# Performance work log

Measured on AMD Instinct MI355X. Metric: run time of the kernel, lower is better.

Reference implementation:

```python
import jax, jax.numpy as jnp
import numpy as np

B, L, H = 64, 512, 400          # batch, seq_len, encoder hidden (HeadSentinel(400))
EN, EL, NLAB = 256, 128, 128    # edge-node dim, edge-label hidden, num head_tags


def setup_inputs():
    key = jax.random.key(0)
    ks = jax.random.split(key, 16)
    g = lambda k, shape, s=0.05: jax.random.normal(k, shape, jnp.float32) * s
    return dict(
        memory_bank=jax.random.normal(ks[0], (B, L, H), jnp.float32),
        edge_heads=jax.random.randint(ks[1], (B, L), 0, L + 1, jnp.int32),
        edge_labels=jax.random.randint(ks[2], (B, L), 0, NLAB, jnp.int32),
        corefs=jax.random.randint(ks[3], (B, L), 0, L, jnp.int32),
        mask=jnp.ones((B, L), jnp.int32),
        sentinel=g(ks[4], (H,)),
        W_enh=g(ks[5], (H, EN)), b_enh=jnp.zeros((EN,), jnp.float32),
        W_enm=g(ks[6], (H, EN)), b_enm=jnp.zeros((EN,), jnp.float32),
        W_elh=g(ks[7], (H, EL)), b_elh=jnp.zeros((EL,), jnp.float32),
        W_elm=g(ks[8], (H, EL)), b_elm=jnp.zeros((EL,), jnp.float32),
        ba_U=g(ks[9], (EN, EN)), ba_Wd=g(ks[10], (EN,)), ba_We=g(ks[11], (EN,)),
        ba_b=jnp.zeros((), jnp.float32),
        lbl_U=g(ks[12], (NLAB, EL, EL)), lbl_Wl=g(ks[13], (NLAB, EL)),
        lbl_Wr=g(ks[14], (NLAB, EL)), lbl_b=jnp.zeros((NLAB,), jnp.float32),
    )


def _label_scores(elh_sel, elm, lbl_U, lbl_Wl, lbl_Wr, lbl_b):
    # Bilinear label scorer: [B, L1, NLAB]
    return (jnp.einsum('bld,nde,ble->bln', elh_sel, lbl_U, elm)
            + elh_sel @ lbl_Wl.T + elm @ lbl_Wr.T + lbl_b)


def reference(memory_bank, edge_heads, edge_labels, corefs, mask, sentinel,
              W_enh, b_enh, W_enm, b_enm, W_elh, b_elh, W_elm, b_elm,
              ba_U, ba_Wd, ba_We, ba_b, lbl_U, lbl_Wl, lbl_Wr, lbl_b):
    elu = jax.nn.elu
    Bsz = memory_bank.shape[0]
    # ---- add head sentinel (mask/heads/labels get a leading zero column) ----
    mb = jnp.concatenate([jnp.broadcast_to(sentinel, (Bsz, 1, sentinel.shape[0])), memory_bank], 1)
    z = jnp.zeros((Bsz, 1), jnp.int32)
    heads1 = jnp.concatenate([z, edge_heads], 1)    # [B, L1]
    labels1 = jnp.concatenate([z, edge_labels], 1)  # [B, L1]
    mask1 = jnp.concatenate([z, mask], 1)           # [B, L1]
    L1 = mb.shape[1]
    # ---- encode (Dropout is identity at inference) ----
    enh = elu(mb @ W_enh + b_enh)
    enm = elu(mb @ W_enm + b_enm)
    elh = elu(mb @ W_elh + b_elh)
    elm = elu(mb @ W_elm + b_elm)
    # ---- biaffine edge-node scores: s[b, head, mod] ----
    node_scores = (jnp.einsum('bhd,de,bme->bhm', enh, ba_U, enm)
                   + (enh @ ba_Wd)[:, :, None] + (enm @ ba_We)[:, None, :] + ba_b)
    # ---- loss ----
    mask2 = (mask1[:, :, None] + mask1[:, None, :]).astype(jnp.float32)
    node_ll = jax.nn.log_softmax(node_scores + jnp.log(mask2 + 1e-45), axis=1)
    elh_gold = jnp.take_along_axis(elh, heads1[:, :, None], axis=1)  # gather_nd(create_indices)
    lbl_ll = jax.nn.log_softmax(_label_scores(elh_gold, elm, lbl_U, lbl_Wl, lbl_Wr, lbl_b), axis=2)
    gold_node_ll = jnp.take_along_axis(node_ll, heads1[:, None, :], axis=1)[:, 0, :]  # ll[b, head[b,m], m]
    gold_lbl_ll = jnp.take_along_axis(lbl_ll, labels1[:, :, None], axis=2)[:, :, 0]   # ll[b, m, label[b,m]]
    node_nll = -jnp.sum(gold_node_ll[:, 1:])
    label_nll = -jnp.sum(gold_lbl_ll[:, 1:])
    # ---- decode ----
    dec = node_scores + jnp.diag(jnp.full((L1,), -jnp.inf))
    mm = (1.0 - mask1.astype(jnp.float32)) * (-1e8)
    dec = dec + mm[:, :, None] + mm[:, None, :]
    pred_heads = jnp.argmax(dec, axis=1)                              # [B, L1]
    elh_pred = jnp.take_along_axis(elh, pred_heads[:, :, None], axis=1)
    pred_lbl = jnp.max(_label_scores(elh_pred, elm, lbl_U, lbl_Wl, lbl_Wr, lbl_b), axis=2)
    return (pred_heads[:, 1:].astype(jnp.float32), pred_lbl[:, 1:],
            labels1.astype(jnp.float32), node_nll, label_nll)
```

## Files before the change

### kernel.cpp

```cpp
#include <hip/hip_runtime.h>
#include <hip/hip_bf16.h>

#define BB 64
#define LLEN 512
#define HH 400
#define L1 513
#define TT 32832
#define NE 768
#define KP 16640
#define PHW 4160
#define KPAD 416

typedef __attribute__((ext_vector_type(4))) float f32x4;
typedef __attribute__((ext_vector_type(8))) short bf16x8;
typedef unsigned int u32;
typedef __attribute__((address_space(1))) const u32* gptr_t;
typedef __attribute__((address_space(3))) u32* sptr_t;

__device__ inline unsigned short f2bf(float x){
  unsigned u = __float_as_uint(x);
  unsigned r = (u + 0x7fffu + ((u >> 16) & 1u)) >> 16;
  return (unsigned short)r;
}
__device__ inline unsigned cvtpk(float a, float b){
  unsigned r;
  asm("v_cvt_pk_bf16_f32 %0, %1, %2" : "=v"(r) : "v"(a), "v"(b));
  return r;
}
__device__ inline float bf2f(unsigned short h){
  return __uint_as_float(((unsigned)h) << 16);
}

__global__ __launch_bounds__(256) void k_init(const int* eh, const int* el, float* out,
                                              int* idx, int* labbuf){
  int t = blockIdx.x*256 + threadIdx.x;
  if (t < TT){
    int b = t / L1, m = t - b*L1;
    int lab = m ? el[b*LLEN + m - 1] : 0;
    int hd  = m ? eh[b*LLEN + m - 1] : 0;
    out[65536 + t] = (float)lab;
    labbuf[t] = lab;
    idx[t] = b*L1 + hd;
  }
  if (blockIdx.x == 0 && threadIdx.x < 2) out[98368 + threadIdx.x] = 0.f;
}

__global__ __launch_bounds__(256) void k_wcat(const float* Wenh,const float* benh,
    const float* Wenm,const float* benm,const float* Welh,const float* belh,
    const float* Welm,const float* belm, unsigned short* WH, unsigned short* WL,
    float* bcat){
  int g = blockIdx.x*256 + threadIdx.x;
  if (g < NE*KPAD){
    int n = g / KPAD, k = g - n*KPAD;
    float v = 0.f;
    if (k < HH){
      if (n < 256) v = Wenh[k*256 + n];
      else if (n < 512) v = Wenm[k*256 + n - 256];
      else if (n < 640) v = Welh[k*128 + n - 512];
      else v = Welm[k*128 + n - 640];
    }
    unsigned short h = f2bf(v);
    WH[g] = h;
    WL[g] = f2bf(v - bf2f(h));
  }
  if (g < NE){
    float v;
    if (g < 256) v = benh[g];
    else if (g < 512) v = benm[g - 256];
    else if (g < 640) v = belh[g - 512];
    else v = belm[g - 640];
    bcat[g] = v;
  }
}

__global__ __launch_bounds__(256) void k_wu(const float* baU, unsigned short* UH,
    unsigned short* UL){
  int g = blockIdx.x*256 + threadIdx.x;
  int n = g >> 8, k = g & 255;
  float v = baU[k*256 + n];
  unsigned short h = f2bf(v);
  UH[g] = h;
  UL[g] = f2bf(v - bf2f(h));
}

__global__ __launch_bounds__(256) void k_wtt(const float* lblU, const float* Wl,
    const float* Wr, unsigned short* WtTp){
  int n = blockIdx.y;
  int kp = blockIdx.x*256 + threadIdx.x;
  if (kp >= KP) return;
  int p = kp / PHW; int q2 = kp - p*PHW; int dd = q2 >> 5; int j = q2 & 31; int e = p*32 + j;
  float v;
  if (dd < 128) v = lblU[(size_t)n*16384 + dd*128 + e];
  else if (dd == 128) v = Wl[n*128 + e];
  else v = Wr[n*128 + e];
  WtTp[(size_t)n*KP + kp] = f2bf(v);
}

__global__ __launch_bounds__(512) void k_encm(const float* mb, const float* sent,
    const unsigned short* WH, const unsigned short* WL, const float* bcat, float* E){
  __shared__ __align__(16) unsigned char Bst[2][2][8192];
  int tid = threadIdx.x, w = tid >> 6, lane = tid & 63, c = lane & 15, q = lane >> 4;
  int tb0 = blockIdx.x*256 + w*32;
  int n0 = blockIdx.y*128;

  const float* ap[2];
  #pragma unroll
  for (int ms = 0; ms < 2; ms++){
    int row = tb0 + ms*16 + c;
    const float* p = sent;
    if (row < TT){
      int br = row / L1, mr = row - br*L1;
      if (mr) p = mb + (size_t)(br*LLEN + mr - 1)*HH;
    }
    ap[ms] = p;
  }

  int f = tid;
  int bn = ((f >> 6) << 4) + (f & 15);
  int bkq = (f >> 4) & 3;
  const char* srcH = (const char*)WH + (size_t)(n0 + bn)*(KPAD*2) + bkq*16;
  const char* srcL = (const char*)WL + (size_t)(n0 + bn)*(KPAD*2) + bkq*16;
  auto stageB = [&](int s){
    __builtin_amdgcn_global_load_lds((gptr_t)(srcH + (size_t)s*64),
        (sptr_t)(&Bst[s & 1][0][f*16]), 16, 0, 0);
    __builtin_amdgcn_global_load_lds((gptr_t)(srcL + (size_t)s*64),
        (sptr_t)(&Bst[s & 1][1][f*16]), 16, 0, 0);
  };

  float4 a0[2], a1[2];
  auto loadA = [&](int s){
    #pragma unroll
    for (int ms = 0; ms < 2; ms++){
      int k = s*32 + q*8;
      float4 v0 = make_float4(0.f,0.f,0.f,0.f), v1 = v0;
      if (k < HH){ v0 = *(const float4*)(ap[ms] + k); v1 = *(const float4*)(ap[ms] + k + 4); }
      a0[ms] = v0; a1[ms] = v1;
    }
  };
  stageB(0);
  loadA(0);

  f32x4 acc[2][8];
  #pragma unroll
  for (int ms = 0; ms < 2; ms++)
    #pragma unroll
    for (int ns = 0; ns < 8; ns++){ acc[ms][ns][0]=0.f; acc[ms][ns][1]=0.f; acc[ms][ns][2]=0.f; acc[ms][ns][3]=0.f; }

  for (int s = 0; s < 13; s++){
    asm volatile("s_waitcnt vmcnt(0)" ::: "memory");
    __builtin_amdgcn_sched_barrier(0);
    __builtin_amdgcn_s_barrier();
    __builtin_amdgcn_sched_barrier(0);
    if (s + 1 < 13) stageB(s + 1);
    bf16x8 Ah[2], Al[2];
    #pragma unroll
    for (int ms = 0; ms < 2; ms++){
      float v[8] = {a0[ms].x,a0[ms].y,a0[ms].z,a0[ms].w,a1[ms].x,a1[ms].y,a1[ms].z,a1[ms].w};
      union { unsigned u[4]; bf16x8 b; } uh, ul;
      float r[8];
      #pragma unroll
      for (int j = 0; j < 4; j++){
        unsigned h = cvtpk(v[2*j], v[2*j+1]);
        uh.u[j] = h;
        r[2*j]   = v[2*j]   - __uint_as_float((h & 0xffffu) << 16);
        r[2*j+1] = v[2*j+1] - __uint_as_float((h >> 16) << 16);
      }
      #pragma unroll
      for (int j = 0; j < 4; j++) ul.u[j] = cvtpk(r[2*j], r[2*j+1]);
      Ah[ms] = uh.b; Al[ms] = ul.b;
    }
    if (s + 1 < 13) loadA(s + 1);
    const char* bh = (const char*)&Bst[s & 1][0][0];
    const char* bl = (const char*)&Bst[s & 1][1][0];
    #pragma unroll
    for (int ns = 0; ns < 8; ns++){
      bf16x8 BH = *(const bf16x8*)(bh + ns*1024 + lane*16);
      bf16x8 BL = *(const bf16x8*)(bl + ns*1024 + lane*16);
      #pragma unroll
      for (int ms = 0; ms < 2; ms++){
        acc[ms][ns] = __builtin_amdgcn_mfma_f32_16x16x32_bf16(Ah[ms], BH, acc[ms][ns], 0, 0, 0);
        acc[ms][ns] = __builtin_amdgcn_mfma_f32_16x16x32_bf16(Ah[ms], BL, acc[ms][ns], 0, 0, 0);
        acc[ms][ns] = __builtin_amdgcn_mfma_f32_16x16x32_bf16(Al[ms], BH, acc[ms][ns], 0, 0, 0);
      }
    }
  }

  float bvv[8];
  #pragma unroll
  for (int ns = 0; ns < 8; ns++) bvv[ns] = bcat[n0 + ns*16 + c];
  #pragma unroll
  for (int ms = 0; ms < 2; ms++){
    #pragma unroll
    for (int i = 0; i < 4; i++){
      int row = tb0 + ms*16 + 4*q + i;
      if (row < TT){
        #pragma unroll
        for (int ns = 0; ns < 8; ns++){
          float t = acc[ms][ns][i] + bvv[ns];
          E[(size_t)row*NE + n0 + ns*16 + c] = t > 0.f ? t : expm1f(t);
        }
      }
    }
  }
}

__global__ __launch_bounds__(256) void k_t1m(const float* E, const unsigned short* UH,
    const unsigned short* UL, float* T1){
  __shared__ __align__(16) unsigned char Bst[2][2][8192];
  int tid = threadIdx.x, w = tid >> 6, lane = tid & 63, c = lane & 15, q = lane >> 4;
  int tb0 = blockIdx.x*128 + w*32;
  int n0 = blockIdx.y*128;

  const float* ap[2];
  #pragma unroll
  for (int ms = 0; ms < 2; ms++){
    int row = tb0 + ms*16 + c;
    ap[ms] = E + (size_t)(row < TT ? row : 0)*NE;
  }

  auto stageB = [&](int s){
    #pragma unroll
    for (int i = 0; i < 2; i++){
      int f = i*256 + tid;
      int n = n0 + ((f >> 6) << 4) + (f & 15);
      int kq = (f >> 4) & 3;
      __builtin_amdgcn_global_load_lds((gptr_t)((const char*)UH + (size_t)n*512 + (size_t)s*64 + kq*16),
          (sptr_t)(&Bst[s & 1][0][f*16]), 16, 0, 0);
      __builtin_amdgcn_global_load_lds((gptr_t)((const char*)UL + (size_t)n*512 + (size_t)s*64 + kq*16),
          (sptr_t)(&Bst[s & 1][1][f*16]), 16, 0, 0);
    }
  };

  float4 a0[2], a1[2];
  auto loadA = [&](int s){
    #pragma unroll
    for (int ms = 0; ms < 2; ms++){
      int k = s*32 + q*8;
      a0[ms] = *(const float4*)(ap[ms] + k);
      a1[ms] = *(const float4*)(ap[ms] + k + 4);
    }
  };
  stageB(0);
  loadA(0);

  f32x4 acc[2][8];
  #pragma unroll
  for (int ms = 0; ms < 2; ms++)
    #pragma unroll
    for (int ns = 0; ns < 8; ns++){ acc[ms][ns][0]=0.f; acc[ms][ns][1]=0.f; acc[ms][ns][2]=0.f; acc[ms][ns][3]=0.f; }

  for (int s = 0; s < 8; s++){
    asm volatile("s_waitcnt vmcnt(0)" ::: "memory");
    __builtin_amdgcn_sched_barrier(0);
    __builtin_amdgcn_s_barrier();
    __builtin_amdgcn_sched_barrier(0);
    if (s + 1 < 8) stageB(s + 1);
    bf16x8 Ah[2], Al[2];
    #pragma unroll
    for (int ms = 0; ms < 2; ms++){
      float v[8] = {a0[ms].x,a0[ms].y,a0[ms].z,a0[ms].w,a1[ms].x,a1[ms].y,a1[ms].z,a1[ms].w};
      union { unsigned u[4]; bf16x8 b; } uh, ul;
      float r[8];
      #pragma unroll
      for (int j = 0; j < 4; j++){
        unsigned h = cvtpk(v[2*j], v[2*j+1]);
        uh.u[j] = h;
        r[2*j]   = v[2*j]   - __uint_as_float((h & 0xffffu) << 16);
        r[2*j+1] = v[2*j+1] - __uint_as_float((h >> 16) << 16);
      }
      #pragma unroll
      for (int j = 0; j < 4; j++) ul.u[j] = cvtpk(r[2*j], r[2*j+1]);
      Ah[ms] = uh.b; Al[ms] = ul.b;
    }
    if (s + 1 < 8) loadA(s + 1);
    const char* bh = (const char*)&Bst[s & 1][0][0];
    const char* bl = (const char*)&Bst[s & 1][1][0];
    #pragma unroll
    for (int ns = 0; ns < 8; ns++){
      bf16x8 BH = *(const bf16x8*)(bh + ns*1024 + lane*16);
      bf16x8 BL = *(const bf16x8*)(bl + ns*1024 + lane*16);
      #pragma unroll
      for (int ms = 0; ms < 2; ms++){
        acc[ms][ns] = __builtin_amdgcn_mfma_f32_16x16x32_bf16(Ah[ms], BH, acc[ms][ns], 0, 0, 0);
        acc[ms][ns] = __builtin_amdgcn_mfma_f32_16x16x32_bf16(Ah[ms], BL, acc[ms][ns], 0, 0, 0);
        acc[ms][ns] = __builtin_amdgcn_mfma_f32_16x16x32_bf16(Al[ms], BH, acc[ms][ns], 0, 0, 0);
      }
    }
  }

  #pragma unroll
  for (int ms = 0; ms < 2; ms++){
    #pragma unroll
    for (int i = 0; i < 4; i++){
      int row = tb0 + ms*16 + 4*q + i;
      if (row < TT){
        #pragma unroll
        for (int ns = 0; ns < 8; ns++)
          T1[(size_t)row*256 + n0 + ns*16 + c] = acc[ms][ns][i];
      }
    }
  }
}

__global__ __launch_bounds__(256) void k_vecs(const float* E, const float* Wd,
    const float* We, const float* bab, float* dvec, float* evec){
  int w = threadIdx.x >> 6, lane = threadIdx.x & 63;
  int t = blockIdx.x*4 + w;
  const float* enh = E + (size_t)t*NE;
  const float* enm = enh + 256;
  float sd = 0.f, se = 0.f;
  for (int l = lane; l < 256; l += 64){ sd += enh[l]*Wd[l]; se += enm[l]*We[l]; }
  for (int o = 1; o < 64; o <<= 1){ sd += __shfl_xor(sd, o, 64); se += __shfl_xor(se, o, 64); }
  if (lane == 0){ dvec[t] = sd + bab[0]; evec[t] = se; }
}

__global__ __launch_bounds__(256) void k_nsm(const float* T1, const float* E,
    const float* dvec, const float* evec, float* S){
  __shared__ __align__(16) unsigned char Bst[2][2][8192];
  int tid = threadIdx.x, w = tid >> 6, lane = tid & 63, c = lane & 15, q = lane >> 4;
  int b = blockIdx.y;
  int tm = blockIdx.x / 5, tn = blockIdx.x - tm*5;
  int Mb = tm*128, n0 = tn*128;
  int tb0 = Mb + w*32;

  const float* ap[2];
  #pragma unroll
  for (int ms = 0; ms < 2; ms++){
    int h = tb0 + ms*16 + c;
    int hc = h < L1 ? h : L1 - 1;
    ap[ms] = T1 + ((size_t)b*L1 + hc)*256;
  }

  auto stageB = [&](int s, int buf){
    int k0 = s*32;
    #pragma unroll
    for (int i = 0; i < 2; i++){
      int f = i*256 + tid;
      int mc = n0 + ((f >> 6) << 4) + (f & 15);
      int kq = (f >> 4) & 3;
      int mcc = mc < L1 ? mc : L1 - 1;
      const float* src = E + ((size_t)b*L1 + mcc)*NE + 256 + k0 + kq*8;
      float4 v0 = *(const float4*)src;
      float4 v1 = *(const float4*)(src + 4);
      float v[8] = {v0.x,v0.y,v0.z,v0.w,v1.x,v1.y,v1.z,v1.w};
      union { unsigned u[4]; uint4 u4; } uh, ul;
      float r[8];
      #pragma unroll
      for (int j = 0; j < 4; j++){
        unsigned h = cvtpk(v[2*j], v[2*j+1]);
        uh.u[j] = h;
        r[2*j]   = v[2*j]   - __uint_as_float((h & 0xffffu) << 16);
        r[2*j+1] = v[2*j+1] - __uint_as_float((h >> 16) << 16);
      }
      #pragma unroll
      for (int j = 0; j < 4; j++) ul.u[j] = cvtpk(r[2*j], r[2*j+1]);
      *(uint4*)&Bst[buf][0][f*16] = uh.u4;
      *(uint4*)&Bst[buf][1][f*16] = ul.u4;
    }
  };

  float4 a0[2], a1[2];
  auto loadA = [&](int s){
    #pragma unroll
    for (int ms = 0; ms < 2; ms++){
      int k = s*32 + q*8;
      a0[ms] = *(const float4*)(ap[ms] + k);
      a1[ms] = *(const float4*)(ap[ms] + k + 4);
    }
  };

  stageB(0, 0);
  loadA(0);

  f32x4 acc[2][8];
  #pragma unroll
  for (int ms = 0; ms < 2; ms++)
    #pragma unroll
    for (int ns = 0; ns < 8; ns++){ acc[ms][ns][0]=0.f; acc[ms][ns][1]=0.f; acc[ms][ns][2]=0.f; acc[ms][ns][3]=0.f; }

  __syncthreads();

  for (int s = 0; s < 8; s++){
    if (s + 1 < 8) stageB(s + 1, (s + 1) & 1);
    bf16x8 Ah[2], Al[2];
    #pragma unroll
    for (int ms = 0; ms < 2; ms++){
      float v[8] = {a0[ms].x,a0[ms].y,a0[ms].z,a0[ms].w,a1[ms].x,a1[ms].y,a1[ms].z,a1[ms].w};
      union { unsigned u[4]; bf16x8 b; } uh, ul;
      float r[8];
      #pragma unroll
      for (int j = 0; j < 4; j++){
        unsigned h = cvtpk(v[2*j], v[2*j+1]);
        uh.u[j] = h;
        r[2*j]   = v[2*j]   - __uint_as_float((h & 0xffffu) << 16);
        r[2*j+1] = v[2*j+1] - __uint_as_float((h >> 16) << 16);
      }
      #pragma unroll
      for (int j = 0; j < 4; j++) ul.u[j] = cvtpk(r[2*j], r[2*j+1]);
      Ah[ms] = uh.b; Al[ms] = ul.b;
    }
    if (s + 1 < 8) loadA(s + 1);
    const char* bh = (const char*)&Bst[s & 1][0][0];
    const char* bl = (const char*)&Bst[s & 1][1][0];
    #pragma unroll
    for (int ns = 0; ns < 8; ns++){
      bf16x8 BH = *(const bf16x8*)(bh + ns*1024 + lane*16);
      bf16x8 BL = *(const bf16x8*)(bl + ns*1024 + lane*16);
      #pragma unroll
      for (int ms = 0; ms < 2; ms++){
        acc[ms][ns] = __builtin_amdgcn_mfma_f32_16x16x32_bf16(Ah[ms], BH, acc[ms][ns], 0, 0, 0);
        acc[ms][ns] = __builtin_amdgcn_mfma_f32_16x16x32_bf16(Ah[ms], BL, acc[ms][ns], 0, 0, 0);
        acc[ms][ns] = __builtin_amdgcn_mfma_f32_16x16x32_bf16(Al[ms], BH, acc[ms][ns], 0, 0, 0);
      }
    }
    __syncthreads();
  }

  float er[8];
  #pragma unroll
  for (int ns = 0; ns < 8; ns++){
    int m = n0 + ns*16 + c;
    er[ns] = (m < L1) ? evec[b*L1 + m] : 0.f;
  }
  float* Sb = S + (size_t)b*L1*L1;
  #pragma unroll
  for (int ms = 0; ms < 2; ms++){
    #pragma unroll
    for (int i = 0; i < 4; i++){
      int h = tb0 + ms*16 + 4*q + i;
      if (h < L1){
        float dv = dvec[b*L1 + h];
        #pragma unroll
        for (int ns = 0; ns < 8; ns++){
          int m = n0 + ns*16 + c;
          if (m < L1) Sb[(size_t)h*L1 + m] = acc[ms][ns][i] + dv + er[ns];
        }
      }
    }
  }
}

__global__ __launch_bounds__(256) void k_nodecol(const float* S, const int* eh,
    const int* mask, float* out, int* idx){
  int b = blockIdx.y, mt = blockIdx.x;
  __shared__ float msk[L1];
  __shared__ float rM[8][32], rS[8][32], rG[8][32], rB[8][32];
  __shared__ int rH[8][32];
  __shared__ float npart[32];
  int tid = threadIdx.x; int c = tid & 31, r = tid >> 5;
  for (int h = tid; h < L1; h += 256) msk[h] = h ? (float)mask[b*LLEN + h - 1] : 0.f;
  __syncthreads();
  int m = mt*32 + c; bool valid = m < L1; int mc = valid ? m : (L1-1);
  float maskm = msk[mc];
  int gold = 0; if (valid && m) gold = eh[b*LLEN + m - 1];
  const float* Sb = S + (size_t)b*L1*L1;
  float Mx = -3.4e38f, Sm = 0.f, G = 0.f, Bv = -3.4e38f; int Bh = 0;
  for (int h = r; h < L1; h += 8){
    float s = Sb[(size_t)h*L1 + mc];
    float adj = s + ((msk[h] + maskm) > 1.5f ? 0.69314718055994531f : 0.f);
    float nm = fmaxf(Mx, adj);
    Sm = Sm * expf(Mx - nm) + expf(adj - nm);
    Mx = nm;
    if (h == gold) G = adj;
    float dv = (h == m) ? -3.4e38f : (s + (msk[h] > 0.5f ? 0.f : -1e8f));
    if (dv > Bv){ Bv = dv; Bh = h; }
  }
  rM[r][c] = Mx; rS[r][c] = Sm; rG[r][c] = G; rB[r][c] = Bv; rH[r][c] = Bh;
  __syncthreads();
  if (r == 0){
    float M0 = rM[0][c], S0 = rS[0][c], G0 = rG[0][c], B0 = rB[0][c]; int H0 = rH[0][c];
    for (int rr = 1; rr < 8; rr++){
      float m2 = rM[rr][c], s2 = rS[rr][c];
      float nm = fmaxf(M0, m2);
      S0 = S0*expf(M0 - nm) + s2*expf(m2 - nm); M0 = nm;
      G0 += rG[rr][c];
      float b2 = rB[rr][c]; int h2 = rH[rr][c];
      if (b2 > B0 || (b2 == B0 && h2 < H0)){ B0 = b2; H0 = h2; }
    }
    float nll = 0.f;
    if (valid && m >= 1) nll = (M0 + logf(S0)) - G0;
    npart[c] = nll;
    if (valid){
      idx[TT + b*L1 + m] = b*L1 + H0;
      if (m >= 1) out[b*LLEN + m - 1] = (float)H0;
    }
  }
  __syncthreads();
  if (tid == 0){
    float ssum = 0.f;
    for (int i2 = 0; i2 < 32; i2++) ssum += npart[i2];
    atomicAdd(out + 98368, ssum);
  }
}

__global__ __launch_bounds__(512, 1) void k_label(const float* E, const unsigned short* WtTp,
    const int* idx, const int* labbuf, const float* lblb, float* out){
  __shared__ __align__(16) unsigned char Bst[8*8192];
  __shared__ __align__(16) unsigned int xls[256*65];
  int tid = threadIdx.x;
  int w = tid >> 6, lane = tid & 63, c = lane & 15, q = lane >> 4;
  int wgrp = w & 3, khalf = w >> 2;
  int bx = blockIdx.x;
  bool pred = bx >= 128;
  int q0 = (bx & 127) * 256;
  int ibase = pred ? TT : 0;

  const char* gW = (const char*)WtTp;
  int f = tid;
  int bn = ((f >> 6) << 4) + (f & 15);
  int bkq = (f >> 4) & 3;
  const char* bsrc0 = gW + (size_t)bn*(KP*2) + (size_t)bkq*16;
  unsigned char* BbA = Bst;
  unsigned char* BbB = Bst + 4*8192;
  auto stage2 = [&](int s){
    __builtin_amdgcn_global_load_lds((gptr_t)(bsrc0 + (size_t)s*64),
        (sptr_t)(BbA + (s & 3)*8192 + f*16), 16, 0, 0);
    __builtin_amdgcn_global_load_lds((gptr_t)(bsrc0 + (size_t)(260 + s)*64),
        (sptr_t)(BbB + (s & 3)*8192 + f*16), 16, 0, 0);
  };
  stage2(0); stage2(1);

  {
    int tok = tid >> 1, half = tid & 1;
    int qq = q0 + tok;
    int trow = (qq >> 9)*L1 + (qq & 511) + 1;
    int g = idx[ibase + trow];
    const float* xr = E + (size_t)g*NE + 512 + half*64;
    unsigned* dstx = &xls[tok*65 + half*32];
    #pragma unroll
    for (int j = 0; j < 16; j++){
      float4 v = *(const float4*)(xr + j*4);
      dstx[2*j]   = cvtpk(v.x, v.y);
      dstx[2*j+1] = cvtpk(v.z, v.w);
    }
  }

  const float *yvb[4], *xvb[4];
  int tokl[4];
  #pragma unroll
  for (int ms = 0; ms < 4; ms++){
    int tl = (wgrp*4 + ms)*16 + c;
    tokl[ms] = tl;
    int qq = q0 + tl;
    int trow = (qq >> 9)*L1 + (qq & 511) + 1;
    int g = idx[ibase + trow];
    yvb[ms] = E + (size_t)trow*NE + 640 + 8*q;
    xvb[ms] = E + (size_t)g*NE + 512 + 8*q;
  }
  f32x4 acc[4][8];
  #pragma unroll
  for (int ms = 0; ms < 4; ms++)
    #pragma unroll
    for (int ns = 0; ns < 8; ns++){ acc[ms][ns][0]=0.f; acc[ms][ns][1]=0.f; acc[ms][ns][2]=0.f; acc[ms][ns][3]=0.f; }

  __syncthreads();

  const unsigned short* xsh = (const unsigned short*)xls;
  float xs0[4], xs1[4];
  #pragma unroll
  for (int ms = 0; ms < 4; ms++){
    xs0[ms] = bf2f(xsh[tokl[ms]*130]);
    xs1[ms] = bf2f(xsh[tokl[ms]*130 + 1]);
  }

  float yreg[4][8];
  for (int u = 0; u < 130; u++){
    if (u) { asm volatile("s_waitcnt vmcnt(0)" ::: "memory"); }
    __builtin_amdgcn_sched_barrier(0);
    __builtin_amdgcn_s_barrier();
    __builtin_amdgcn_sched_barrier(0);
    if (2*u + 2 < 260){ stage2(2*u + 2); stage2(2*u + 3); }
    int ph = (u >= 65);
    int d0 = 2*u - ph*130;
    if (d0 == 0){
      int e0 = (khalf*2 + ph) * 32;
      #pragma unroll
      for (int ms = 0; ms < 4; ms++){
        float4 v0 = *(const float4*)(yvb[ms] + e0);
        float4 v1 = *(const float4*)(yvb[ms] + e0 + 4);
        yreg[ms][0]=v0.x; yreg[ms][1]=v0.y; yreg[ms][2]=v0.z; yreg[ms][3]=v0.w;
        yreg[ms][4]=v1.x; yreg[ms][5]=v1.y; yreg[ms][6]=v1.z; yreg[ms][7]=v1.w;
      }
    }
    bf16x8 afr0[4], afr1[4];
    if (d0 < 128){
      #pragma unroll
      for (int ms = 0; ms < 4; ms++){
        float a0 = xs0[ms], a1 = xs1[ms];
        union { unsigned u[4]; bf16x8 v; } u0, u1;
        u0.u[0] = cvtpk(a0*yreg[ms][0], a0*yreg[ms][1]);
        u0.u[1] = cvtpk(a0*yreg[ms][2], a0*yreg[ms][3]);
        u0.u[2] = cvtpk(a0*yreg[ms][4], a0*yreg[ms][5]);
        u0.u[3] = cvtpk(a0*yreg[ms][6], a0*yreg[ms][7]);
        u1.u[0] = cvtpk(a1*yreg[ms][0], a1*yreg[ms][1]);
        u1.u[1] = cvtpk(a1*yreg[ms][2], a1*yreg[ms][3]);
        u1.u[2] = cvtpk(a1*yreg[ms][4], a1*yreg[ms][5]);
        u1.u[3] = cvtpk(a1*yreg[ms][6], a1*yreg[ms][7]);
        afr0[ms] = u0.v; afr1[ms] = u1.v;
      }
    } else {
      int e0 = (khalf*2 + ph) * 32;
      #pragma unroll
      for (int ms = 0; ms < 4; ms++){
        float4 u0f = *(const float4*)(xvb[ms] + e0);
        float4 u1f = *(const float4*)(xvb[ms] + e0 + 4);
        union { unsigned u[4]; bf16x8 v; } ux, uy;
        ux.u[0]=cvtpk(u0f.x,u0f.y); ux.u[1]=cvtpk(u0f.z,u0f.w);
        ux.u[2]=cvtpk(u1f.x,u1f.y); ux.u[3]=cvtpk(u1f.z,u1f.w);
        uy.u[0]=cvtpk(yreg[ms][0],yreg[ms][1]); uy.u[1]=cvtpk(yreg[ms][2],yreg[ms][3]);
        uy.u[2]=cvtpk(yreg[ms][4],yreg[ms][5]); uy.u[3]=cvtpk(yreg[ms][6],yreg[ms][7]);
        afr0[ms] = ux.v; afr1[ms] = uy.v;
      }
    }
    {
      int nd0 = 2*(u + 1) - ((u + 1 >= 65) ? 130 : 0);
      if (nd0 >= 128) nd0 = 0;
      #pragma unroll
      for (int ms = 0; ms < 4; ms++){
        xs0[ms] = bf2f(xsh[tokl[ms]*130 + nd0]);
        xs1[ms] = bf2f(xsh[tokl[ms]*130 + nd0 + 1]);
      }
    }
    const char* hb = (const char*)(khalf ? BbB : BbA);
    const char* bs0 = hb + ((2*u) & 3)*8192;
    const char* bs1 = hb + ((2*u + 1) & 3)*8192;
    #pragma unroll
    for (int ns = 0; ns < 8; ns++){
      bf16x8 bfr0 = *(const bf16x8*)(bs0 + ns*1024 + lane*16);
      bf16x8 bfr1 = *(const bf16x8*)(bs1 + ns*1024 + lane*16);
      #pragma unroll
      for (int ms = 0; ms < 4; ms++){
        acc[ms][ns] = __builtin_amdgcn_mfma_f32_16x16x32_bf16(afr0[ms], bfr0, acc[ms][ns], 0, 0, 0);
        acc[ms][ns] = __builtin_amdgcn_mfma_f32_16x16x32_bf16(afr1[ms], bfr1, acc[ms][ns], 0, 0, 0);
      }
    }
  }

  __syncthreads();
  float* cmb = (float*)xls;
  #pragma unroll
  for (int ms = 0; ms < 4; ms++){
    if (khalf == 1){
      #pragma unroll
      for (int ns = 0; ns < 8; ns++)
        *(f32x4*)&cmb[((wgrp*64 + lane)*8 + ((ns + lane) & 7))*4] = acc[ms][ns];
    }
    __syncthreads();
    if (khalf == 0){
      #pragma unroll
      for (int ns = 0; ns < 8; ns++){
        f32x4 t = *(const f32x4*)&cmb[((wgrp*64 + lane)*8 + ((ns + lane) & 7))*4];
        acc[ms][ns][0] += t[0]; acc[ms][ns][1] += t[1];
        acc[ms][ns][2] += t[2]; acc[ms][ns][3] += t[3];
      }
    }
    __syncthreads();
  }
  if (khalf == 1) return;

  float bv[8];
  #pragma unroll
  for (int ns = 0; ns < 8; ns++) bv[ns] = lblb[ns*16 + c];
  float part = 0.f;
  #pragma unroll
  for (int ms = 0; ms < 4; ms++){
    int tb = (wgrp*4 + ms)*16 + 4*q;
    float mx[4] = {-3.4e38f, -3.4e38f, -3.4e38f, -3.4e38f};
    #pragma unroll
    for (int ns = 0; ns < 8; ns++)
      #pragma unroll
      for (int i = 0; i < 4; i++){
        float v = acc[ms][ns][i] + bv[ns];
        mx[i] = fmaxf(mx[i], v);
      }
    #pragma unroll
    for (int o = 1; o < 16; o <<= 1)
      #pragma unroll
      for (int i = 0; i < 4; i++) mx[i] = fmaxf(mx[i], __shfl_xor(mx[i], o, 64));
    if (!pred){
      int lab[4];
      #pragma unroll
      for (int i = 0; i < 4; i++){
        int qq = q0 + tb + i;
        int trow = (qq >> 9)*L1 + (qq & 511) + 1;
        lab[i] = labbuf[trow];
      }
      float se[4] = {0.f,0.f,0.f,0.f}, gp[4] = {0.f,0.f,0.f,0.f};
      #pragma unroll
      for (int ns = 0; ns < 8; ns++)
        #pragma unroll
        for (int i = 0; i < 4; i++){
          float v = acc[ms][ns][i] + bv[ns];
          se[i] += expf(v - mx[i]);
          if (ns*16 + c == lab[i]) gp[i] += v;
        }
      #pragma unroll
      for (int o = 1; o < 16; o <<= 1)
        #pragma unroll
        for (int i = 0; i < 4; i++){ se[i] += __shfl_xor(se[i], o, 64); gp[i] += __shfl_xor(gp[i], o, 64); }
      if (c == 0){
        #pragma unroll
        for (int i = 0; i < 4; i++) part += mx[i] + logf(se[i]) - gp[i];
      }
    } else {
      if (c == 0){
        #pragma unroll
        for (int i = 0; i < 4; i++)
          out[32768 + q0 + tb + i] = mx[i];
      }
    }
  }
  if (!pred){
    for (int o = 1; o < 64; o <<= 1) part += __shfl_xor(part, o, 64);
    if (lane == 0) atomicAdd(out + 98369, part);
  }
}

extern "C" void kernel_launch(void* const* d_in, const int* in_sizes, int n_in,
                              void* d_out, int out_size, void* d_ws, size_t ws_size,
                              hipStream_t stream){
  const float* memory_bank = (const float*)d_in[0];
  const int* edge_heads = (const int*)d_in[1];
  const int* edge_labels = (const int*)d_in[2];
  const int* mask = (const int*)d_in[4];
  const float* sentinel = (const float*)d_in[5];
  const float* W_enh = (const float*)d_in[6];  const float* b_enh = (const float*)d_in[7];
  const float* W_enm = (const float*)d_in[8];  const float* b_enm = (const float*)d_in[9];
  const float* W_elh = (const float*)d_in[10]; const float* b_elh = (const float*)d_in[11];
  const float* W_elm = (const float*)d_in[12]; const float* b_elm = (const float*)d_in[13];
  const float* ba_U = (const float*)d_in[14];  const float* ba_Wd = (const float*)d_in[15];
  const float* ba_We = (const float*)d_in[16]; const float* ba_b = (const float*)d_in[17];
  const float* lbl_U = (const float*)d_in[18]; const float* lbl_Wl = (const float*)d_in[19];
  const float* lbl_Wr = (const float*)d_in[20]; const float* lbl_b = (const float*)d_in[21];
  float* out = (float*)d_out;

  char* wsc = (char*)d_ws;
  size_t o = 0;
  auto alloc = [&](size_t n){ o = (o + 255) & ~(size_t)255; void* pp = wsc + o; o += n; return pp; };
  float* E     = (float*)alloc((size_t)TT*NE*4);
  float* T1    = (float*)alloc((size_t)TT*256*4);
  float* S     = (float*)alloc((size_t)BB*L1*L1*4);
  unsigned short* WH = (unsigned short*)alloc((size_t)NE*KPAD*2);
  unsigned short* WL = (unsigned short*)alloc((size_t)NE*KPAD*2);
  unsigned short* UH = (unsigned short*)alloc((size_t)256*256*2);
  unsigned short* UL = (unsigned short*)alloc((size_t)256*256*2);
  float* bcat  = (float*)alloc((size_t)NE*4);
  unsigned short* WtTp = (unsigned short*)alloc((size_t)128*KP*2);
  float* dvec  = (float*)alloc((size_t)TT*4);
  float* evec  = (float*)alloc((size_t)TT*4);
  int*   idx   = (int*)alloc((size_t)2*TT*4);
  int*   labbuf= (int*)alloc((size_t)TT*4);

  k_init<<<dim3(129), 256, 0, stream>>>(edge_heads, edge_labels, out, idx, labbuf);
  k_wcat<<<dim3(1248), 256, 0, stream>>>(W_enh, b_enh, W_enm, b_enm, W_elh, b_elh, W_elm, b_elm, WH, WL, bcat);
  k_wu<<<dim3(256), 256, 0, stream>>>(ba_U, UH, UL);
  k_wtt<<<dim3(65, 128), 256, 0, stream>>>(lbl_U, lbl_Wl, lbl_Wr, WtTp);
  k_encm<<<dim3(129, 6), 512, 0, stream>>>(memory_bank, sentinel, WH, WL, bcat, E);
  k_t1m<<<dim3(257, 2), 256, 0, stream>>>(E, UH, UL, T1);
  k_vecs<<<dim3(8208), 256, 0, stream>>>(E, ba_Wd, ba_We, ba_b, dvec, evec);
  k_nsm<<<dim3(25, 64), 256, 0, stream>>>(T1, E, dvec, evec, S);
  k_nodecol<<<dim3(17, 64), 256, 0, stream>>>(S, edge_heads, mask, out, idx);
  k_label<<<dim3(256), 512, 0, stream>>>(E, WtTp, idx, labbuf, lbl_b, out);
}
```

Before: 699.9 us.

## Fuse d/e vector dots into encoder epilogue and transpose score matrix for column reductions

```diff
diff --git a/kernel.cpp b/kernel.cpp
--- a/kernel.cpp
+++ b/kernel.cpp
@@ -32,7 +32,8 @@
 }
 
 __global__ __launch_bounds__(256) void k_init(const int* eh, const int* el, float* out,
-                                              int* idx, int* labbuf){
+                                              int* idx, int* labbuf, const float* bab,
+                                              float* dvec, float* evec){
   int t = blockIdx.x*256 + threadIdx.x;
   if (t < TT){
     int b = t / L1, m = t - b*L1;
@@ -41,6 +42,8 @@
     out[65536 + t] = (float)lab;
     labbuf[t] = lab;
     idx[t] = b*L1 + hd;
+    dvec[t] = bab[0];
+    evec[t] = 0.f;
   }
   if (blockIdx.x == 0 && threadIdx.x < 2) out[98368 + threadIdx.x] = 0.f;
 }
@@ -97,7 +100,8 @@
 }
 
 __global__ __launch_bounds__(512) void k_encm(const float* mb, const float* sent,
-    const unsigned short* WH, const unsigned short* WL, const float* bcat, float* E){
+    const unsigned short* WH, const unsigned short* WL, const float* bcat,
+    const float* Wd, const float* We, float* dvec, float* evec, float* E){
   __shared__ __align__(16) unsigned char Bst[2][2][8192];
   int tid = threadIdx.x, w = tid >> 6, lane = tid & 63, c = lane & 15, q = lane >> 4;
   int tb0 = blockIdx.x*256 + w*32;
@@ -185,6 +189,16 @@
     }
   }
 
+  int yb = blockIdx.y;
+  bool isD = yb < 2, isE = (yb >= 2 && yb < 4);
+  float wv[8];
+  if (isD){
+    #pragma unroll
+    for (int ns = 0; ns < 8; ns++) wv[ns] = Wd[n0 + ns*16 + c];
+  } else if (isE){
+    #pragma unroll
+    for (int ns = 0; ns < 8; ns++) wv[ns] = We[n0 - 256 + ns*16 + c];
+  }
   float bvv[8];
   #pragma unroll
   for (int ns = 0; ns < 8; ns++) bvv[ns] = bcat[n0 + ns*16 + c];
@@ -193,12 +207,20 @@
     #pragma unroll
     for (int i = 0; i < 4; i++){
       int row = tb0 + ms*16 + 4*q + i;
+      float p = 0.f;
       if (row < TT){
         #pragma unroll
         for (int ns = 0; ns < 8; ns++){
           float t = acc[ms][ns][i] + bvv[ns];
-          E[(size_t)row*NE + n0 + ns*16 + c] = t > 0.f ? t : expm1f(t);
+          float e = t > 0.f ? t : expm1f(t);
+          E[(size_t)row*NE + n0 + ns*16 + c] = e;
+          if (isD || isE) p += e * wv[ns];
         }
+      }
+      if (isD || isE){
+        #pragma unroll
+        for (int o = 1; o < 16; o <<= 1) p += __shfl_xor(p, o, 64);
+        if (c == 0 && row < TT) atomicAdd((isD ? dvec : evec) + row, p);
       }
     }
   }
@@ -302,20 +324,8 @@
   }
 }
 
-__global__ __launch_bounds__(256) void k_vecs(const float* E, const float* Wd,
-    const float* We, const float* bab, float* dvec, float* evec){
-  int w = threadIdx.x >> 6, lane = threadIdx.x & 63;
-  int t = blockIdx.x*4 + w;
-  const float* enh = E + (size_t)t*NE;
-  const float* enm = enh + 256;
-  float sd = 0.f, se = 0.f;
-  for (int l = lane; l < 256; l += 64){ sd += enh[l]*Wd[l]; se += enm[l]*We[l]; }
-  for (int o = 1; o < 64; o <<= 1){ sd += __shfl_xor(sd, o, 64); se += __shfl_xor(se, o, 64); }
-  if (lane == 0){ dvec[t] = sd + bab[0]; evec[t] = se; }
-}
-
 __global__ __launch_bounds__(256) void k_nsm(const float* T1, const float* E,
-    const float* dvec, const float* evec, float* S){
+    const float* dvec, const float* evec, float* ST){
   __shared__ __align__(16) unsigned char Bst[2][2][8192];
   int tid = threadIdx.x, w = tid >> 6, lane = tid & 63, c = lane & 15, q = lane >> 4;
   int b = blockIdx.y;
@@ -422,74 +432,87 @@
     int m = n0 + ns*16 + c;
     er[ns] = (m < L1) ? evec[b*L1 + m] : 0.f;
   }
-  float* Sb = S + (size_t)b*L1*L1;
+  float* STb = ST + (size_t)b*L1*L1;
   #pragma unroll
   for (int ms = 0; ms < 2; ms++){
-    #pragma unroll
-    for (int i = 0; i < 4; i++){
-      int h = tb0 + ms*16 + 4*q + i;
-      if (h < L1){
-        float dv = dvec[b*L1 + h];
+    int hb = tb0 + ms*16 + 4*q;
+    if (hb < L1){
+      bool full = (hb + 3 < L1);
+      float dv[4];
+      if (full){
+        float4 d4 = *(const float4*)&dvec[b*L1 + hb];
+        dv[0]=d4.x; dv[1]=d4.y; dv[2]=d4.z; dv[3]=d4.w;
+      } else {
         #pragma unroll
-        for (int ns = 0; ns < 8; ns++){
-          int m = n0 + ns*16 + c;
-          if (m < L1) Sb[(size_t)h*L1 + m] = acc[ms][ns][i] + dv + er[ns];
+        for (int i = 0; i < 4; i++) dv[i] = (hb + i < L1) ? dvec[b*L1 + hb + i] : 0.f;
+      }
+      #pragma unroll
+      for (int ns = 0; ns < 8; ns++){
+        int m = n0 + ns*16 + c;
+        if (m < L1){
+          f32x4 o;
+          #pragma unroll
+          for (int i = 0; i < 4; i++) o[i] = acc[ms][ns][i] + dv[i] + er[ns];
+          if (full) *(f32x4*)&STb[(size_t)m*L1 + hb] = o;
+          else {
+            #pragma unroll
+            for (int i = 0; i < 4; i++) if (hb + i < L1) STb[(size_t)m*L1 + hb + i] = o[i];
+          }
         }
       }
     }
   }
 }
 
-__global__ __launch_bounds__(256) void k_nodecol(const float* S, const int* eh,
+__global__ __launch_bounds__(256) void k_nodecol(const float* ST, const int* eh,
     const int* mask, float* out, int* idx){
-  int b = blockIdx.y, mt = blockIdx.x;
+  int b = blockIdx.y;
+  int tid = threadIdx.x, w = tid >> 6, lane = tid & 63;
   __shared__ float msk[L1];
-  __shared__ float rM[8][32], rS[8][32], rG[8][32], rB[8][32];
-  __shared__ int rH[8][32];
-  __shared__ float npart[32];
-  int tid = threadIdx.x; int c = tid & 31, r = tid >> 5;
+  __shared__ float npart[4];
   for (int h = tid; h < L1; h += 256) msk[h] = h ? (float)mask[b*LLEN + h - 1] : 0.f;
   __syncthreads();
-  int m = mt*32 + c; bool valid = m < L1; int mc = valid ? m : (L1-1);
+  int m = blockIdx.x*4 + w;
+  bool valid = m < L1; int mc = valid ? m : (L1-1);
   float maskm = msk[mc];
   int gold = 0; if (valid && m) gold = eh[b*LLEN + m - 1];
-  const float* Sb = S + (size_t)b*L1*L1;
-  float Mx = -3.4e38f, Sm = 0.f, G = 0.f, Bv = -3.4e38f; int Bh = 0;
-  for (int h = r; h < L1; h += 8){
-    float s = Sb[(size_t)h*L1 + mc];
-    float adj = s + ((msk[h] + maskm) > 1.5f ? 0.69314718055994531f : 0.f);
-    float nm = fmaxf(Mx, adj);
-    Sm = Sm * expf(Mx - nm) + expf(adj - nm);
-    Mx = nm;
-    if (h == gold) G = adj;
-    float dv = (h == m) ? -3.4e38f : (s + (msk[h] > 0.5f ? 0.f : -1e8f));
-    if (dv > Bv){ Bv = dv; Bh = h; }
-  }
-  rM[r][c] = Mx; rS[r][c] = Sm; rG[r][c] = G; rB[r][c] = Bv; rH[r][c] = Bh;
-  __syncthreads();
-  if (r == 0){
-    float M0 = rM[0][c], S0 = rS[0][c], G0 = rG[0][c], B0 = rB[0][c]; int H0 = rH[0][c];
-    for (int rr = 1; rr < 8; rr++){
-      float m2 = rM[rr][c], s2 = rS[rr][c];
-      float nm = fmaxf(M0, m2);
-      S0 = S0*expf(M0 - nm) + s2*expf(m2 - nm); M0 = nm;
-      G0 += rG[rr][c];
-      float b2 = rB[rr][c]; int h2 = rH[rr][c];
-      if (b2 > B0 || (b2 == B0 && h2 < H0)){ B0 = b2; H0 = h2; }
-    }
-    float nll = 0.f;
-    if (valid && m >= 1) nll = (M0 + logf(S0)) - G0;
-    npart[c] = nll;
+  const float* Sm = ST + ((size_t)b*L1 + mc)*L1;
+  float Mx = -3.4e38f, Smm = 0.f, G = 0.f, Bv = -3.4e38f; int Bh = 0;
+  #pragma unroll
+  for (int k = 0; k < 9; k++){
+    int h = lane + 64*k;
+    if (h < L1){
+      float s = Sm[h];
+      float adj = s + ((msk[h] + maskm) > 1.5f ? 0.69314718055994531f : 0.f);
+      float nm = fmaxf(Mx, adj);
+      Smm = Smm * expf(Mx - nm) + expf(adj - nm);
+      Mx = nm;
+      if (h == gold) G = adj;
+      float dv = (h == m) ? -3.4e38f : (s + (msk[h] > 0.5f ? 0.f : -1e8f));
+      if (dv > Bv){ Bv = dv; Bh = h; }
+    }
+  }
+  for (int o = 1; o < 64; o <<= 1){
+    float M2 = __shfl_xor(Mx, o, 64), S2 = __shfl_xor(Smm, o, 64);
+    float nm = fmaxf(Mx, M2);
+    Smm = Smm*expf(Mx - nm) + S2*expf(M2 - nm); Mx = nm;
+    G += __shfl_xor(G, o, 64);
+    float B2 = __shfl_xor(Bv, o, 64); int H2 = __shfl_xor(Bh, o, 64);
+    if (B2 > Bv || (B2 == Bv && H2 < Bh)){ Bv = B2; Bh = H2; }
+  }
+  float nll = 0.f;
+  if (valid && m >= 1) nll = (Mx + logf(Smm)) - G;
+  if (lane == 0){
+    npart[w] = nll;
     if (valid){
-      idx[TT + b*L1 + m] = b*L1 + H0;
-      if (m >= 1) out[b*LLEN + m - 1] = (float)H0;
+      idx[TT + b*L1 + m] = b*L1 + Bh;
+      if (m >= 1) out[b*LLEN + m - 1] = (float)Bh;
     }
   }
   __syncthreads();
   if (tid == 0){
-    float ssum = 0.f;
-    for (int i2 = 0; i2 < 32; i2++) ssum += npart[i2];
-    atomicAdd(out + 98368, ssum);
+    float s4 = npart[0] + npart[1] + npart[2] + npart[3];
+    if (s4 != 0.f) atomicAdd(out + 98368, s4);
   }
 }
 
@@ -624,6 +647,7 @@
     const char* hb = (const char*)(khalf ? BbB : BbA);
     const char* bs0 = hb + ((2*u) & 3)*8192;
     const char* bs1 = hb + ((2*u + 1) & 3)*8192;
+    __builtin_amdgcn_s_setprio(1);
     #pragma unroll
     for (int ns = 0; ns < 8; ns++){
       bf16x8 bfr0 = *(const bf16x8*)(bs0 + ns*1024 + lane*16);
@@ -634,6 +658,7 @@
         acc[ms][ns] = __builtin_amdgcn_mfma_f32_16x16x32_bf16(afr1[ms], bfr1, acc[ms][ns], 0, 0, 0);
       }
     }
+    __builtin_amdgcn_s_setprio(0);
   }
 
   __syncthreads();
@@ -739,7 +764,7 @@
   auto alloc = [&](size_t n){ o = (o + 255) & ~(size_t)255; void* pp = wsc + o; o += n; return pp; };
   float* E     = (float*)alloc((size_t)TT*NE*4);
   float* T1    = (float*)alloc((size_t)TT*256*4);
-  float* S     = (float*)alloc((size_t)BB*L1*L1*4);
+  float* ST    = (float*)alloc((size_t)BB*L1*L1*4);
   unsigned short* WH = (unsigned short*)alloc((size_t)NE*KPAD*2);
   unsigned short* WL = (unsigned short*)alloc((size_t)NE*KPAD*2);
   unsigned short* UH = (unsigned short*)alloc((size_t)256*256*2);
@@ -751,14 +776,13 @@
   int*   idx   = (int*)alloc((size_t)2*TT*4);
   int*   labbuf= (int*)alloc((size_t)TT*4);
 
-  k_init<<<dim3(129), 256, 0, stream>>>(edge_heads, edge_labels, out, idx, labbuf);
+  k_init<<<dim3(129), 256, 0, stream>>>(edge_heads, edge_labels, out, idx, labbuf, ba_b, dvec, evec);
   k_wcat<<<dim3(1248), 256, 0, stream>>>(W_enh, b_enh, W_enm, b_enm, W_elh, b_elh, W_elm, b_elm, WH, WL, bcat);
   k_wu<<<dim3(256), 256, 0, stream>>>(ba_U, UH, UL);
   k_wtt<<<dim3(65, 128), 256, 0, stream>>>(lbl_U, lbl_Wl, lbl_Wr, WtTp);
-  k_encm<<<dim3(129, 6), 512, 0, stream>>>(memory_bank, sentinel, WH, WL, bcat, E);
+  k_encm<<<dim3(129, 6), 512, 0, stream>>>(memory_bank, sentinel, WH, WL, bcat, ba_Wd, ba_We, dvec, evec, E);
   k_t1m<<<dim3(257, 2), 256, 0, stream>>>(E, UH, UL, T1);
-  k_vecs<<<dim3(8208), 256, 0, stream>>>(E, ba_Wd, ba_We, ba_b, dvec, evec);
-  k_nsm<<<dim3(25, 64), 256, 0, stream>>>(T1, E, dvec, evec, S);
-  k_nodecol<<<dim3(17, 64), 256, 0, stream>>>(S, edge_heads, mask, out, idx);
+  k_nsm<<<dim3(25, 64), 256, 0, stream>>>(T1, E, dvec, evec, ST);
+  k_nodecol<<<dim3(129, 64), 256, 0, stream>>>(ST, edge_heads, mask, out, idx);
   k_label<<<dim3(256), 512, 0, stream>>>(E, WtTp, idx, labbuf, lbl_b, out);
 }
```

New measurement: 769.2 us. +9.9%, slower.
